# Performance work log

Hardware: AMD Instinct MI355X
Metric: run time of the kernel (lower is better)

## Reference

```python
import jax, jax.numpy as jnp
import numpy as np

H = 160       # embed_fea (hidden size, also num_layers of gru3)
C = 200       # input_channels (spectral bands)
NCLS = 16     # n_classes
NCHUNK = 10   # spectral segments
T = C // NCHUNK  # timesteps per segment
BN_EPS = 1e-5


def _gru_scan(x_seq, wih, whh, bih, bhh):
    """Single-layer torch-style GRU over x_seq [T, I] with batch=1. Returns all hidden states [T, H]."""
    xp_all = x_seq @ wih.T + bih  # [T, 3H] precomputed input projections (r|z|n)
    h0 = jnp.zeros((whh.shape[1],), x_seq.dtype)

    def step(h, xp):
        hp = h @ whh.T + bhh
        xr, xz, xn = jnp.split(xp, 3)
        hr, hz, hn = jnp.split(hp, 3)
        r = jax.nn.sigmoid(xr + hr)
        z = jax.nn.sigmoid(xz + hz)
        n = jnp.tanh(xn + r * hn)
        h = (1.0 - z) * n + z * h
        return h, h

    _, hs = jax.lax.scan(step, h0, xp_all)
    return hs


def setup_inputs() -> dict:
    key = jax.random.key(0)
    ks = jax.random.split(key, 22)
    s = 0.1  # weight scale to avoid gate saturation
    f32 = jnp.float32
    d = {}
    d["x"] = jax.random.normal(ks[0], (C,), f32)
    # 10 per-segment GRUs (input_size=1), stacked on leading axis
    d["b_wih"] = jax.random.normal(ks[1], (NCHUNK, 3 * H, 1), f32) * s
    d["b_whh"] = jax.random.normal(ks[2], (NCHUNK, 3 * H, H), f32) * s
    d["b_bih"] = jax.random.normal(ks[3], (NCHUNK, 3 * H), f32) * s
    d["b_bhh"] = jax.random.normal(ks[4], (NCHUNK, 3 * H), f32) * s
    # full-spectrum GRU (input_size=1)
    d["g_wih"] = jax.random.normal(ks[5], (3 * H, 1), f32) * s
    d["g_whh"] = jax.random.normal(ks[6], (3 * H, H), f32) * s
    d["g_bih"] = jax.random.normal(ks[7], (3 * H,), f32) * s
    d["g_bhh"] = jax.random.normal(ks[8], (3 * H,), f32) * s
    # gru3: H-layer stacked GRU (all layers have input size H), stacked on leading axis
    d["g3_wih"] = jax.random.normal(ks[9], (H, 3 * H, H), f32) * s
    d["g3_whh"] = jax.random.normal(ks[10], (H, 3 * H, H), f32) * s
    d["g3_bih"] = jax.random.normal(ks[11], (H, 3 * H), f32) * s
    d["g3_bhh"] = jax.random.normal(ks[12], (H, 3 * H), f32) * s
    # BatchNorm1d (eval mode: running stats)
    d["bn_gamma"] = jax.random.normal(ks[13], (H,), f32) * s + 1.0
    d["bn_beta"] = jax.random.normal(ks[14], (H,), f32) * s
    d["bn_mean"] = jnp.zeros((H,), f32)
    d["bn_var"] = jax.random.uniform(ks[15], (H,), f32) + 0.5
    # heads
    d["fc_w"] = jax.random.normal(ks[16], (NCLS, H), f32) * s
    d["fc_b"] = jax.random.normal(ks[17], (NCLS,), f32) * s
    d["reg_w"] = jax.random.normal(ks[18], (C, H), f32) * s
    d["reg_b"] = jax.random.normal(ks[19], (C,), f32) * s
    return d


def reference(x, b_wih, b_whh, b_bih, b_bhh, g_wih, g_whh, g_bih, g_bhh,
              g3_wih, g3_whh, g3_bih, g3_bhh, bn_gamma, bn_beta, bn_mean, bn_var,
              fc_w, fc_b, reg_w, reg_b):
    # chunk spectrum into 10 segments of T steps, run all 10 branch GRUs in parallel via vmap
    xs = x.reshape(NCHUNK, T, 1)
    branch_hs = jax.vmap(_gru_scan)(xs, b_wih, b_whh, b_bih, b_bhh)  # [10, T, H]
    x_cat = branch_hs[:, -1, :]  # last hidden of each branch -> sequence of length 10 [10, H]

    # gru3: H stacked GRU layers over the 10-step sequence; scan over layers
    def layer_step(seq, p):
        wih, whh, bih, bhh = p
        return _gru_scan(seq, wih, whh, bih, bhh), None

    seq_final, _ = jax.lax.scan(layer_step, x_cat, (g3_wih, g3_whh, g3_bih, g3_bhh))
    x_cat_l = jax.nn.relu(seq_final.mean(axis=0))  # avg_pool1d over full length -> [H]

    # full-spectrum GRU + mean pool
    hs_full = _gru_scan(x.reshape(C, 1), g_wih, g_whh, g_bih, g_bhh)  # [C, H]
    x_l = hs_full.mean(axis=0)  # [H]

    x_new = x_l * x_cat_l  # gating fusion
    xb = (x_new - bn_mean) / jnp.sqrt(bn_var + BN_EPS) * bn_gamma + bn_beta
    xr = jax.nn.relu(xb)
    x_class = (xr @ fc_w.T + fc_b)[None, :]  # [1, NCLS]
    x_rec = (xr @ reg_w.T + reg_b)[None, :]  # [1, C]
    return x_class, x_rec
```

## Files before the change

### kernel.cpp

```cpp
#include <hip/hip_runtime.h>
#include <stdint.h>

#define H      160
#define G3     480
#define NCH    10
#define TCH    20
#define CC     200
#define NCLS   16
#define NLAYERS 160
#define NLEVELS 161
#define NSEQ   (NLEVELS * NCH * H)
#define NT     512
#define NPAIR  64
#define NLAYB  (2*NPAIR)
#define GRID   (NLAYB + NCH + 1)

#define CANARY 0x7fbadbadu

typedef float f4 __attribute__((ext_vector_type(4)));

__device__ float g_seq[NSEQ];

__device__ __forceinline__ float sigm(float x){ return 1.0f / (1.0f + expf(-x)); }

__device__ __forceinline__ void stf(float* p, float v){
  __hip_atomic_store(p, v, __ATOMIC_RELAXED, __HIP_MEMORY_SCOPE_AGENT);
}
__device__ __forceinline__ float ldf(float* p){
  return __hip_atomic_load(p, __ATOMIC_RELAXED, __HIP_MEMORY_SCOPE_AGENT);
}
__device__ __forceinline__ float poll_val(float* p){
  float v;
  do { v = ldf(p); } while (__float_as_uint(v) == CANARY);
  return v;
}

__device__ __forceinline__ float dotq20(const float4* __restrict__ w, int stride,
                                        const float* __restrict__ v){
  float a0 = 0.f, a1 = 0.f;
#pragma unroll
  for (int k = 0; k < 20; k += 2){
    float4 wa = w[k*stride], wb = w[(k+1)*stride];
    f4 va = *(const f4*)(v + 4*k), vb = *(const f4*)(v + 4*k + 4);
    a0 = fmaf(wa.x, va.x, a0); a0 = fmaf(wa.y, va.y, a0);
    a0 = fmaf(wa.z, va.z, a0); a0 = fmaf(wa.w, va.w, a0);
    a1 = fmaf(wb.x, vb.x, a1); a1 = fmaf(wb.y, vb.y, a1);
    a1 = fmaf(wb.z, vb.z, a1); a1 = fmaf(wb.w, vb.w, a1);
  }
  return a0 + a1;
}

#define WH_DECL  f4 w00,w01,w02,w03,w04,w05,w06,w07,w08,w09, \
                    w10,w11,w12,w13,w14,w15,w16,w17,w18,w19
#define WH_LOAD(SRC) do { const f4* ws_ = (const f4*)(SRC); \
  w00=ws_[0]; w01=ws_[1]; w02=ws_[2]; w03=ws_[3]; w04=ws_[4]; \
  w05=ws_[5]; w06=ws_[6]; w07=ws_[7]; w08=ws_[8]; w09=ws_[9]; \
  w10=ws_[10];w11=ws_[11];w12=ws_[12];w13=ws_[13];w14=ws_[14]; \
  w15=ws_[15];w16=ws_[16];w17=ws_[17];w18=ws_[18];w19=ws_[19]; } while(0)
#define WH_PIN() asm volatile("" : \
  "+v"(w00),"+v"(w01),"+v"(w02),"+v"(w03),"+v"(w04), \
  "+v"(w05),"+v"(w06),"+v"(w07),"+v"(w08),"+v"(w09), \
  "+v"(w10),"+v"(w11),"+v"(w12),"+v"(w13),"+v"(w14), \
  "+v"(w15),"+v"(w16),"+v"(w17),"+v"(w18),"+v"(w19))
#define MACP(WA,WB,OFF) do { \
  f4 va_ = *(const f4*)(v_ + (OFF));  f4 vb_ = *(const f4*)(v_ + (OFF) + 4); \
  a0_=fmaf(WA.x,va_.x,a0_); a0_=fmaf(WA.y,va_.y,a0_); \
  a0_=fmaf(WA.z,va_.z,a0_); a0_=fmaf(WA.w,va_.w,a0_); \
  a1_=fmaf(WB.x,vb_.x,a1_); a1_=fmaf(WB.y,vb_.y,a1_); \
  a1_=fmaf(WB.z,vb_.z,a1_); a1_=fmaf(WB.w,vb_.w,a1_); } while(0)
#define WH_DOT80(RES, VBASE) do { const float* v_ = (VBASE); \
  float a0_=0.f, a1_=0.f; \
  MACP(w00,w01,0);  MACP(w02,w03,8);  MACP(w04,w05,16); MACP(w06,w07,24); \
  MACP(w08,w09,32); MACP(w10,w11,40); MACP(w12,w13,48); MACP(w14,w15,56); \
  MACP(w16,w17,64); MACP(w18,w19,72); (RES) = a0_ + a1_; } while(0)

extern "C" __global__ void poison_kernel(){
  int i = threadIdx.x + blockIdx.x * blockDim.x;
  if (i < NSEQ) stf(&g_seq[i], __uint_as_float(CANARY));
}

extern "C" __global__ __launch_bounds__(NT, 1)
void spectral_wave(
  const float* __restrict__ x,
  const float* __restrict__ b_wih, const float* __restrict__ b_whh,
  const float* __restrict__ b_bih, const float* __restrict__ b_bhh,
  const float* __restrict__ g_wih, const float* __restrict__ g_whh,
  const float* __restrict__ g_bih, const float* __restrict__ g_bhh,
  const float* __restrict__ g3_wih, const float* __restrict__ g3_whh,
  const float* __restrict__ g3_bih, const float* __restrict__ g3_bhh,
  const float* __restrict__ bn_gamma, const float* __restrict__ bn_beta,
  const float* __restrict__ bn_mean,  const float* __restrict__ bn_var,
  const float* __restrict__ fc_w, const float* __restrict__ fc_b,
  const float* __restrict__ reg_w, const float* __restrict__ reg_b,
  float* __restrict__ out)
{
  const int tid = threadIdx.x;
  const int bid = blockIdx.x;

  __shared__ float4 s_w4[9600];
  __shared__ __align__(16) float s_buf[1280];

  if (bid < NLAYB) {
    const int p = bid >> 1, role = bid & 1, hbase = role * 80;
    const int nlay = (p < 32) ? 3 : 2;
    const bool act = tid < 480;
    const int j    = tid % 240;
    const int hf   = (tid / 240) & 1;
    const int c0   = 80 * hf;
    const int band = j / 80;
    const int grow = band*160 + (j % 80) + hbase;

    float* sx   = s_buf;
    float* sh   = s_buf + 160;
    float* swp  = s_buf + 320;
    float* shp2 = s_buf + 800;

    for (int li = 0; li < nlay; ++li){
      const int l = p + 64*li;

      {
        const float4* src = (const float4*)(g3_wih + (size_t)l*G3*H);
        for (int it = 0; it < 19; ++it){
          int fidx = it*NT + tid;
          if (fidx < 9600){
            int jj = fidx / 40, qi = fidx - jj*40;
            int gr = (jj/80)*160 + (jj%80) + hbase;
            s_w4[qi*240 + jj] = src[gr*40 + qi];
          }
        }
      }
      WH_DECL;
      float bihj = 0.f, bhhj = 0.f;
      if (act){
        WH_LOAD(g3_whh + ((size_t)l*G3 + grow)*H + c0);
        WH_PIN();
        if (hf == 0){ bihj = g3_bih[l*G3 + grow]; bhhj = g3_bhh[l*G3 + grow]; }
      }
      if (tid < 160) sh[tid] = 0.f;
      __syncthreads();

      float* seq_in  = g_seq + (size_t)l     * NCH * H;
      float* seq_out = g_seq + (size_t)(l+1) * NCH * H;

      for (int t = 0; t < NCH; ++t){
        if (tid < 160){
          sx[tid] = poll_val(&seq_in[t*H + tid]);
        } else if (tid < 240 && t > 0){
          int oi = (role == 0 ? 80 : 0) + (tid - 160);
          sh[oi] = poll_val(&seq_out[(t-1)*H + oi]);
        }
        __syncthreads();
        if (act){
          float s_w = dotq20(&s_w4[hf*4800 + j], 240, sx + c0) + bihj;
          float s_h; WH_DOT80(s_h, sh + c0); s_h += bhhj;
          if (band < 2) swp[hf*240 + j] = s_w + s_h;
          else { swp[hf*240 + j] = s_w; shp2[hf*80 + (j-160)] = s_h; }
        }
        __syncthreads();
        if (tid < 80){
          int i = tid, hi = hbase + i;
          float pr = swp[i]       + swp[240 + i];
          float pz = swp[80 + i]  + swp[320 + i];
          float xn = swp[160 + i] + swp[400 + i];
          float hn = shp2[i]      + shp2[80 + i];
          float rg = sigm(pr);
          float z  = sigm(pz);
          float n  = tanhf(xn + rg * hn);
          float h  = (1.f - z) * n + z * sh[hi];
          sh[hi] = h;
          stf(&seq_out[t*H + hi], h);
        }
      }
      __syncthreads();
    }
  } else if (bid < NLAYB + NCH) {
    const int b = bid - NLAYB;
    const bool act = tid < 480;
    const int rr = tid;
    float* spre = s_buf;
    float* sxn  = s_buf + 320;
    float* shn  = s_buf + 480;
    float* sh   = s_buf + 640;

    {
      const float4* src = (const float4*)(b_whh + (size_t)b*G3*H);
      for (int it = 0; it < 19; ++it){
        int fidx = it*NT + tid;
        if (fidx < 9600){
          int r2 = fidx / 20, k = fidx - r2*20;
          s_w4[k*480 + r2] = src[r2*40 + 20 + k];
        }
      }
    }
    WH_DECL;
    float wij = 0.f, bihj = 0.f, bhhj = 0.f;
    if (act){
      WH_LOAD(b_whh + ((size_t)b*G3 + rr)*H);
      WH_PIN();
      wij  = b_wih[b*G3 + rr];
      bihj = b_bih[b*G3 + rr];
      bhhj = b_bhh[b*G3 + rr];
    }
    if (tid < 160) sh[tid] = 0.f;
    __syncthreads();
    for (int t = 0; t < TCH; ++t){
      float xv = x[b*TCH + t];
      if (act){
        float ahl; WH_DOT80(ahl, sh);
        float ah = bhhj + ahl + dotq20(&s_w4[rr], 480, sh + 80);
        float ax = fmaf(xv, wij, bihj);
        if (rr < 320) spre[rr] = ax + ah;
        else { sxn[rr-320] = ax; shn[rr-320] = ah; }
      }
      __syncthreads();
      if (tid < 160){
        float rg = sigm(spre[tid]);
        float z  = sigm(spre[160 + tid]);
        float n  = tanhf(sxn[tid] + rg * shn[tid]);
        float h  = (1.f - z) * n + z * sh[tid];
        sh[tid] = h;
        if (t == TCH - 1) stf(&g_seq[(size_t)b*H + tid], h);
      }
      __syncthreads();
    }
  } else {
    const bool act = tid < 480;
    const int rr = tid;
    float* spre = s_buf;
    float* sxn  = s_buf + 320;
    float* shn  = s_buf + 480;
    float* sh   = s_buf + 640;

    {
      const float4* src = (const float4*)g_whh;
      for (int it = 0; it < 19; ++it){
        int fidx = it*NT + tid;
        if (fidx < 9600){
          int r2 = fidx / 20, k = fidx - r2*20;
          s_w4[k*480 + r2] = src[r2*40 + 20 + k];
        }
      }
    }
    WH_DECL;
    float wij = 0.f, bihj = 0.f, bhhj = 0.f;
    if (act){
      WH_LOAD(g_whh + (size_t)rr*H);
      WH_PIN();
      wij  = g_wih[rr];
      bihj = g_bih[rr];
      bhhj = g_bhh[rr];
    }
    if (tid < 160) sh[tid] = 0.f;
    __syncthreads();
    float hsum = 0.f;
    for (int t = 0; t < CC; ++t){
      float xv = x[t];
      if (act){
        float ahl; WH_DOT80(ahl, sh);
        float ah = bhhj + ahl + dotq20(&s_w4[rr], 480, sh + 80);
        float ax = fmaf(xv, wij, bihj);
        if (rr < 320) spre[rr] = ax + ah;
        else { sxn[rr-320] = ax; shn[rr-320] = ah; }
      }
      __syncthreads();
      if (tid < 160){
        float rg = sigm(spre[tid]);
        float z  = sigm(spre[160 + tid]);
        float n  = tanhf(sxn[tid] + rg * shn[tid]);
        float h  = (1.f - z) * n + z * sh[tid];
        sh[tid] = h;
        hsum += h;
      }
      __syncthreads();
    }
    if (tid < 160){
      float acc = 0.f;
      float* lvl = g_seq + (size_t)NLAYERS * NCH * H;
      for (int t = 0; t < NCH; ++t) acc += poll_val(&lvl[t*H + tid]);
      float xc   = fmaxf(acc * (1.0f / NCH), 0.f);
      float xl   = hsum * (1.0f / CC);
      float xnew = xl * xc;
      float xbn  = (xnew - bn_mean[tid]) * rsqrtf(bn_var[tid] + 1e-5f)
                   * bn_gamma[tid] + bn_beta[tid];
      spre[tid] = fmaxf(xbn, 0.f);
    }
    __syncthreads();
    if (tid < NCLS + CC){
      const float* wrow; float acc;
      if (tid < NCLS){ wrow = fc_w + (size_t)tid * H; acc = fc_b[tid]; }
      else           { wrow = reg_w + (size_t)(tid - NCLS) * H; acc = reg_b[tid - NCLS]; }
#pragma unroll
      for (int q = 0; q < 40; q++){
        float4 wv = *(const float4*)(wrow + 4*q);
        f4 xv = *(const f4*)(spre + 4*q);
        acc = fmaf(wv.x, xv.x, acc);
        acc = fmaf(wv.y, xv.y, acc);
        acc = fmaf(wv.z, xv.z, acc);
        acc = fmaf(wv.w, xv.w, acc);
      }
      out[tid] = acc;
    }
  }
}

extern "C" void kernel_launch(void* const* d_in, const int* in_sizes, int n_in,
                              void* d_out, int out_size, void* d_ws, size_t ws_size,
                              hipStream_t stream) {
  (void)in_sizes; (void)n_in; (void)out_size; (void)d_ws; (void)ws_size;

  hipLaunchKernelGGL(poison_kernel, dim3((NSEQ + 255)/256), dim3(256), 0, stream);

  hipLaunchKernelGGL(spectral_wave, dim3(GRID), dim3(NT), 0, stream,
    (const float*)d_in[0],
    (const float*)d_in[1],  (const float*)d_in[2],
    (const float*)d_in[3],  (const float*)d_in[4],
    (const float*)d_in[5],  (const float*)d_in[6],
    (const float*)d_in[7],  (const float*)d_in[8],
    (const float*)d_in[9],  (const float*)d_in[10],
    (const float*)d_in[11], (const float*)d_in[12],
    (const float*)d_in[13], (const float*)d_in[14],
    (const float*)d_in[15], (const float*)d_in[16],
    (const float*)d_in[17], (const float*)d_in[18],
    (const float*)d_in[19], (const float*)d_in[20],
    (float*)d_out);
}
```

Baseline: 538.6 us.

## Add XCD-local fast polling buffer, remap layer blocks by XCD, pad LDS stride

```diff
diff --git a/kernel.cpp b/kernel.cpp
--- a/kernel.cpp
+++ b/kernel.cpp
@@ -20,19 +20,36 @@
 typedef float f4 __attribute__((ext_vector_type(4)));
 
 __device__ float g_seq[NSEQ];
+__device__ float g_fast[NSEQ];
 
 __device__ __forceinline__ float sigm(float x){ return 1.0f / (1.0f + expf(-x)); }
 
 __device__ __forceinline__ void stf(float* p, float v){
   __hip_atomic_store(p, v, __ATOMIC_RELAXED, __HIP_MEMORY_SCOPE_AGENT);
 }
+__device__ __forceinline__ void stw(float* p, float v){
+  __hip_atomic_store(p, v, __ATOMIC_RELAXED, __HIP_MEMORY_SCOPE_WORKGROUP);
+}
 __device__ __forceinline__ float ldf(float* p){
   return __hip_atomic_load(p, __ATOMIC_RELAXED, __HIP_MEMORY_SCOPE_AGENT);
 }
-__device__ __forceinline__ float poll_val(float* p){
+__device__ __forceinline__ float ld_sc0(const float* p){
   float v;
-  do { v = ldf(p); } while (__float_as_uint(v) == CANARY);
+  asm volatile("global_load_dword %0, %1, off sc0\n\t"
+               "s_waitcnt vmcnt(0)"
+               : "=v"(v) : "v"(p) : "memory");
   return v;
+}
+__device__ __forceinline__ float poll2(const float* fast, float* slow){
+  while (true){
+#pragma unroll
+    for (int i = 0; i < 4; ++i){
+      float v = ld_sc0(fast);
+      if (__float_as_uint(v) != CANARY) return v;
+    }
+    float v = ldf(slow);
+    if (__float_as_uint(v) != CANARY) return v;
+  }
 }
 
 __device__ __forceinline__ float dotq20(const float4* __restrict__ w, int stride,
@@ -76,7 +93,8 @@
 
 extern "C" __global__ void poison_kernel(){
   int i = threadIdx.x + blockIdx.x * blockDim.x;
-  if (i < NSEQ) stf(&g_seq[i], __uint_as_float(CANARY));
+  float c = __uint_as_float(CANARY);
+  if (i < NSEQ){ stf(&g_seq[i], c); stf(&g_fast[i], c); }
 }
 
 extern "C" __global__ __launch_bounds__(NT, 1)
@@ -97,11 +115,15 @@
   const int tid = threadIdx.x;
   const int bid = blockIdx.x;
 
-  __shared__ float4 s_w4[9600];
+  int lm;
+  if (bid < NLAYB){ int xcd = bid & 7, slot = bid >> 3; lm = xcd*16 + slot; }
+  else lm = bid;
+
+  __shared__ float4 s_w4[9640];
   __shared__ __align__(16) float s_buf[1280];
 
-  if (bid < NLAYB) {
-    const int p = bid >> 1, role = bid & 1, hbase = role * 80;
+  if (lm < NLAYB) {
+    const int p = lm >> 1, role = lm & 1, hbase = role * 80;
     const int nlay = (p < 32) ? 3 : 2;
     const bool act = tid < 480;
     const int j    = tid % 240;
@@ -125,7 +147,7 @@
           if (fidx < 9600){
             int jj = fidx / 40, qi = fidx - jj*40;
             int gr = (jj/80)*160 + (jj%80) + hbase;
-            s_w4[qi*240 + jj] = src[gr*40 + qi];
+            s_w4[qi*241 + jj] = src[gr*40 + qi];
           }
         }
       }
@@ -139,19 +161,21 @@
       if (tid < 160) sh[tid] = 0.f;
       __syncthreads();
 
-      float* seq_in  = g_seq + (size_t)l     * NCH * H;
-      float* seq_out = g_seq + (size_t)(l+1) * NCH * H;
+      float* seq_in   = g_seq  + (size_t)l     * NCH * H;
+      float* seq_out  = g_seq  + (size_t)(l+1) * NCH * H;
+      float* fast_in  = g_fast + (size_t)l     * NCH * H;
+      float* fast_out = g_fast + (size_t)(l+1) * NCH * H;
 
       for (int t = 0; t < NCH; ++t){
         if (tid < 160){
-          sx[tid] = poll_val(&seq_in[t*H + tid]);
+          sx[tid] = poll2(&fast_in[t*H + tid], &seq_in[t*H + tid]);
         } else if (tid < 240 && t > 0){
           int oi = (role == 0 ? 80 : 0) + (tid - 160);
-          sh[oi] = poll_val(&seq_out[(t-1)*H + oi]);
+          sh[oi] = poll2(&fast_out[(t-1)*H + oi], &seq_out[(t-1)*H + oi]);
         }
         __syncthreads();
         if (act){
-          float s_w = dotq20(&s_w4[hf*4800 + j], 240, sx + c0) + bihj;
+          float s_w = dotq20(&s_w4[hf*4820 + j], 241, sx + c0) + bihj;
           float s_h; WH_DOT80(s_h, sh + c0); s_h += bhhj;
           if (band < 2) swp[hf*240 + j] = s_w + s_h;
           else { swp[hf*240 + j] = s_w; shp2[hf*80 + (j-160)] = s_h; }
@@ -168,13 +192,14 @@
           float n  = tanhf(xn + rg * hn);
           float h  = (1.f - z) * n + z * sh[hi];
           sh[hi] = h;
+          stw(&fast_out[t*H + hi], h);
           stf(&seq_out[t*H + hi], h);
         }
       }
       __syncthreads();
     }
-  } else if (bid < NLAYB + NCH) {
-    const int b = bid - NLAYB;
+  } else if (lm < NLAYB + NCH) {
+    const int b = lm - NLAYB;
     const bool act = tid < 480;
     const int rr = tid;
     float* spre = s_buf;
@@ -188,7 +213,7 @@
         int fidx = it*NT + tid;
         if (fidx < 9600){
           int r2 = fidx / 20, k = fidx - r2*20;
-          s_w4[k*480 + r2] = src[r2*40 + 20 + k];
+          s_w4[k*481 + r2] = src[r2*40 + 20 + k];
         }
       }
     }
@@ -207,7 +232,7 @@
       float xv = x[b*TCH + t];
       if (act){
         float ahl; WH_DOT80(ahl, sh);
-        float ah = bhhj + ahl + dotq20(&s_w4[rr], 480, sh + 80);
+        float ah = bhhj + ahl + dotq20(&s_w4[rr], 481, sh + 80);
         float ax = fmaf(xv, wij, bihj);
         if (rr < 320) spre[rr] = ax + ah;
         else { sxn[rr-320] = ax; shn[rr-320] = ah; }
@@ -219,7 +244,10 @@
         float n  = tanhf(sxn[tid] + rg * shn[tid]);
         float h  = (1.f - z) * n + z * sh[tid];
         sh[tid] = h;
-        if (t == TCH - 1) stf(&g_seq[(size_t)b*H + tid], h);
+        if (t == TCH - 1){
+          stw(&g_fast[(size_t)b*H + tid], h);
+          stf(&g_seq[(size_t)b*H + tid], h);
+        }
       }
       __syncthreads();
     }
@@ -237,7 +265,7 @@
         int fidx = it*NT + tid;
         if (fidx < 9600){
           int r2 = fidx / 20, k = fidx - r2*20;
-          s_w4[k*480 + r2] = src[r2*40 + 20 + k];
+          s_w4[k*481 + r2] = src[r2*40 + 20 + k];
         }
       }
     }
@@ -257,7 +285,7 @@
       float xv = x[t];
       if (act){
         float ahl; WH_DOT80(ahl, sh);
-        float ah = bhhj + ahl + dotq20(&s_w4[rr], 480, sh + 80);
+        float ah = bhhj + ahl + dotq20(&s_w4[rr], 481, sh + 80);
         float ax = fmaf(xv, wij, bihj);
         if (rr < 320) spre[rr] = ax + ah;
         else { sxn[rr-320] = ax; shn[rr-320] = ah; }
@@ -275,8 +303,9 @@
     }
     if (tid < 160){
       float acc = 0.f;
-      float* lvl = g_seq + (size_t)NLAYERS * NCH * H;
-      for (int t = 0; t < NCH; ++t) acc += poll_val(&lvl[t*H + tid]);
+      float* lvl  = g_seq  + (size_t)NLAYERS * NCH * H;
+      float* lvlf = g_fast + (size_t)NLAYERS * NCH * H;
+      for (int t = 0; t < NCH; ++t) acc += poll2(&lvlf[t*H + tid], &lvl[t*H + tid]);
       float xc   = fmaxf(acc * (1.0f / NCH), 0.f);
       float xl   = hsum * (1.0f / CC);
       float xnew = xl * xc;
```

After: 556.0 us. 1.03x slower.
